# Kernel tuning notes

Measured on AMD Instinct MI355X. Metric: run time of the kernel, lower is better.

## Reference

```python
import jax, jax.numpy as jnp
import numpy as np

B, NV, JN = 1024, 8, 21
V = NV * JN            # 168 tokens = num_view * joint_num
F_DIM, NH, DQ, DV = 512, 4, 128, 128
HID = 512
EPS = 1e-6
NEG = float(-2**32 + 1)


def _layer_norm(x, g, b):
    mu = jnp.mean(x, axis=-1, keepdims=True)
    var = jnp.mean(jnp.square(x - mu), axis=-1, keepdims=True)
    return (x - mu) * jax.lax.rsqrt(var + EPS) * g + b


def setup_inputs() -> dict:
    key = jax.random.key(0)
    ks = jax.random.split(key, 12)
    s = 0.02
    return {
        "x": jax.random.normal(ks[0], (B, V, F_DIM), dtype=jnp.float32),
        "valid": jax.random.randint(ks[1], (B, NV), 0, 2),
        "wq": jax.random.normal(ks[2], (NH * DQ, F_DIM), dtype=jnp.float32) * s,
        "bq": jnp.zeros((NH * DQ,), dtype=jnp.float32),
        "wk": jax.random.normal(ks[3], (NH * DQ, F_DIM), dtype=jnp.float32) * s,
        "bk": jnp.zeros((NH * DQ,), dtype=jnp.float32),
        "wv": jax.random.normal(ks[4], (NH * DV, F_DIM), dtype=jnp.float32) * s,
        "bv": jnp.zeros((NH * DV,), dtype=jnp.float32),
        "fc_w": jax.random.normal(ks[5], (F_DIM, NH * DV), dtype=jnp.float32) * s,
        "fc_b": jnp.zeros((F_DIM,), dtype=jnp.float32),
        "ln1_g": jnp.ones((F_DIM,), dtype=jnp.float32),
        "ln1_b": jnp.zeros((F_DIM,), dtype=jnp.float32),
        "ln2_g": jnp.ones((F_DIM,), dtype=jnp.float32),
        "ln2_b": jnp.zeros((F_DIM,), dtype=jnp.float32),
        "fc1_w": jax.random.normal(ks[6], (HID, F_DIM), dtype=jnp.float32) * s,
        "fc1_b": jnp.zeros((HID,), dtype=jnp.float32),
        "fc2_w": jax.random.normal(ks[7], (F_DIM, HID), dtype=jnp.float32) * s,
        "fc2_b": jnp.zeros((F_DIM,), dtype=jnp.float32),
    }


def reference(x, valid, wq, bq, wk, bk, wv, bv, fc_w, fc_b,
              ln1_g, ln1_b, ln2_g, ln2_b, fc1_w, fc1_b, fc2_w, fc2_b):
    bs = x.shape[0]
    h = _layer_norm(x, ln1_g, ln1_b)                          # [B,V,f]
    q = (h @ wq.T + bq).reshape(bs, V, NH, DQ)                # [B,V,H,dq]
    k = (h @ wk.T + bk).reshape(bs, V, NH, DQ)
    v = (h @ wv.T + bv).reshape(bs, V, NH, DV)
    attn = jnp.einsum('bqhd,bkhd->bhqk', q, k) / jnp.sqrt(jnp.float32(DQ))
    # valid mask: per-view validity expanded to per-token, pairwise additive
    w = jnp.where(valid == 0, NEG, 0.0).astype(x.dtype)       # [B,NV]
    w = jnp.repeat(w, JN, axis=1)                             # [B,V], view-major
    m = w[:, :, None] + w[:, None, :]                         # [B,V,V]
    attn = attn + m[:, None, :, :]
    attn = jax.nn.softmax(attn, axis=-1)
    out = jnp.einsum('bhqk,bkhd->bqhd', attn, v).reshape(bs, V, NH * DV)
    out = out @ fc_w.T + fc_b
    x = x + out
    # MLP residual block
    h2 = _layer_norm(x, ln2_g, ln2_b)
    h2 = jax.nn.relu(h2 @ fc1_w.T + fc1_b) @ fc2_w.T + fc2_b
    return x + h2
```

## Files before the change

kernel.cpp:

```cpp
#include <hip/hip_runtime.h>
#include <stdint.h>

#define BATCH 1024
#define NVIEW 8
#define JN_   21
#define VTOK  168
#define FDIM  512
#define NHEAD 4
#define DHEAD 128
#define MROWS (BATCH*VTOK)
#define SCALE2 0.127517434f

typedef __attribute__((ext_vector_type(8))) short s8v;
typedef __attribute__((ext_vector_type(4))) short s4v;
typedef __attribute__((ext_vector_type(4))) float f4v;

static __device__ __forceinline__ short f2bf(float f){
  unsigned u = __builtin_bit_cast(unsigned, f);
  unsigned r = (u + 0x7FFFu + ((u >> 16) & 1u)) >> 16;
  return (short)(unsigned short)r;
}
static __device__ __forceinline__ float bf2f(short s){
  unsigned u = ((unsigned)(unsigned short)s) << 16;
  return __builtin_bit_cast(float, u);
}

#define GL16(gp, lp) __builtin_amdgcn_global_load_lds( \
    (__attribute__((address_space(1))) void*)(gp), \
    (__attribute__((address_space(3))) void*)(lp), 16, 0, 0)

__global__ __launch_bounds__(256) void convert_w(
    const float* __restrict__ wq, const float* __restrict__ wk,
    const float* __restrict__ wv, const float* __restrict__ fcw,
    const float* __restrict__ fc1, const float* __restrict__ fc2,
    short* __restrict__ dst){
  int id = blockIdx.x * 256 + threadIdx.x;
  int e = id * 4;
  int seg = e >> 18;
  int off = e & 262143;
  const float* s = seg==0?wq: seg==1?wk: seg==2?wv: seg==3?fcw: seg==4?fc1: fc2;
  float4 u = *(const float4*)(s + off);
  s4v o; o[0]=f2bf(u.x); o[1]=f2bf(u.y); o[2]=f2bf(u.z); o[3]=f2bf(u.w);
  *(s4v*)(dst + e) = o;
}

__global__ __launch_bounds__(256) void ln1_kernel(
    const float* __restrict__ x, const float* __restrict__ g,
    const float* __restrict__ bb, short* __restrict__ h){
  int row  = blockIdx.x * 4 + (threadIdx.x >> 6);
  int lane = threadIdx.x & 63;
  size_t base = (size_t)row * 512 + lane * 8;
  float4 u0 = *(const float4*)(x + base);
  float4 u1 = *(const float4*)(x + base + 4);
  float s = u0.x+u0.y+u0.z+u0.w + u1.x+u1.y+u1.z+u1.w;
  float q = u0.x*u0.x+u0.y*u0.y+u0.z*u0.z+u0.w*u0.w
          + u1.x*u1.x+u1.y*u1.y+u1.z*u1.z+u1.w*u1.w;
  #pragma unroll
  for (int o = 1; o < 64; o <<= 1){ s += __shfl_xor(s,o); q += __shfl_xor(q,o); }
  float mu = s * (1.f/512.f);
  float rstd = rsqrtf(q*(1.f/512.f) - mu*mu + 1e-6f);
  float4 g0 = *(const float4*)(g + lane*8),  g1 = *(const float4*)(g + lane*8 + 4);
  float4 b0 = *(const float4*)(bb + lane*8), b1 = *(const float4*)(bb + lane*8 + 4);
  s8v o_;
  o_[0]=f2bf((u0.x-mu)*rstd*g0.x+b0.x); o_[1]=f2bf((u0.y-mu)*rstd*g0.y+b0.y);
  o_[2]=f2bf((u0.z-mu)*rstd*g0.z+b0.z); o_[3]=f2bf((u0.w-mu)*rstd*g0.w+b0.w);
  o_[4]=f2bf((u1.x-mu)*rstd*g1.x+b1.x); o_[5]=f2bf((u1.y-mu)*rstd*g1.y+b1.y);
  o_[6]=f2bf((u1.z-mu)*rstd*g1.z+b1.z); o_[7]=f2bf((u1.w-mu)*rstd*g1.w+b1.w);
  *(s8v*)(h + base) = o_;
}

__global__ __launch_bounds__(256) void resid_ln(
    const float* __restrict__ x, const short* __restrict__ y,
    const float* __restrict__ g, const float* __restrict__ bb,
    short* __restrict__ g2){
  int row  = blockIdx.x * 4 + (threadIdx.x >> 6);
  int lane = threadIdx.x & 63;
  size_t base = (size_t)row * 512 + lane * 8;
  float4 u0 = *(const float4*)(x + base);
  float4 u1 = *(const float4*)(x + base + 4);
  s8v yv = *(const s8v*)(y + base);
  float v[8];
  v[0]=u0.x+bf2f(yv[0]); v[1]=u0.y+bf2f(yv[1]); v[2]=u0.z+bf2f(yv[2]); v[3]=u0.w+bf2f(yv[3]);
  v[4]=u1.x+bf2f(yv[4]); v[5]=u1.y+bf2f(yv[5]); v[6]=u1.z+bf2f(yv[6]); v[7]=u1.w+bf2f(yv[7]);
  float s = 0.f, q = 0.f;
  #pragma unroll
  for (int i = 0; i < 8; i++){ s += v[i]; q += v[i]*v[i]; }
  #pragma unroll
  for (int o = 1; o < 64; o <<= 1){ s += __shfl_xor(s,o); q += __shfl_xor(q,o); }
  float mu = s * (1.f/512.f);
  float rstd = rsqrtf(q*(1.f/512.f) - mu*mu + 1e-6f);
  float4 g0 = *(const float4*)(g + lane*8),  g1 = *(const float4*)(g + lane*8 + 4);
  float4 b0 = *(const float4*)(bb + lane*8), b1 = *(const float4*)(bb + lane*8 + 4);
  s8v o_;
  o_[0]=f2bf((v[0]-mu)*rstd*g0.x+b0.x); o_[1]=f2bf((v[1]-mu)*rstd*g0.y+b0.y);
  o_[2]=f2bf((v[2]-mu)*rstd*g0.z+b0.z); o_[3]=f2bf((v[3]-mu)*rstd*g0.w+b0.w);
  o_[4]=f2bf((v[4]-mu)*rstd*g1.x+b1.x); o_[5]=f2bf((v[5]-mu)*rstd*g1.y+b1.y);
  o_[6]=f2bf((v[6]-mu)*rstd*g1.z+b1.z); o_[7]=f2bf((v[7]-mu)*rstd*g1.w+b1.w);
  *(s8v*)(g2 + base) = o_;
}

template<int MODE>
__global__ __launch_bounds__(512) void gemm_bt(
    const short* __restrict__ A, const short* __restrict__ Bm,
    const float* __restrict__ bias0, const float* __restrict__ bias1,
    const float* __restrict__ aux, short* __restrict__ out0,
    short* __restrict__ out1, float* __restrict__ outf){
  __shared__ short As[3][16384];
  __shared__ short Bs[3][8192];
  int tid = threadIdx.x, lane = tid & 63;
  int wid = tid >> 6, wr = wid >> 1, wc = wid & 1;
  int lg = lane >> 4, l15 = lane & 15;
  int nwg  = gridDim.x * gridDim.y;
  int flat = blockIdx.y * gridDim.x + blockIdx.x;
  int cpx  = nwg >> 3;
  int swz  = (flat & 7) * cpx + (flat >> 3);
  int bx = swz % gridDim.x, by = swz / gridDim.x;
  size_t mt, nt;
  if (MODE == 1){ mt = bx; nt = by; }
  else          { nt = bx; mt = by; }
  size_t m0 = mt * 256, n0 = nt * 128;
  const short* Ab = A + m0 * 512;
  const short* Bb = Bm + n0 * 512;
  f4v zf = {0.f,0.f,0.f,0.f};
  f4v acc[4][4];
  #pragma unroll
  for (int m=0;m<4;m++)
    #pragma unroll
    for (int n=0;n<4;n++) acc[m][n] = zf;

#define STAGE_T(bufi, kt) do {                                        \
    _Pragma("unroll")                                                 \
    for (int r_ = 0; r_ < 4; r_++){                                   \
      int c_ = r_*512 + tid;                                          \
      int row_ = c_ >> 3;                                             \
      int chk_ = (c_ & 7) ^ (row_ & 7);                               \
      GL16(Ab + (size_t)row_*512 + (kt) + chk_*8, &As[bufi][c_*8]);   \
    }                                                                 \
    _Pragma("unroll")                                                 \
    for (int r_ = 0; r_ < 2; r_++){                                   \
      int c_ = r_*512 + tid;                                          \
      int row_ = c_ >> 3;                                             \
      int chk_ = (c_ & 7) ^ (row_ & 7);                               \
      GL16(Bb + (size_t)row_*512 + (kt) + chk_*8, &Bs[bufi][c_*8]);   \
    }                                                                 \
  } while(0)

  STAGE_T(0, 0); STAGE_T(1, 64); STAGE_T(2, 128);

  #pragma unroll
  for (int t = 0; t < 8; ++t){
    if (t < 6)       asm volatile("s_waitcnt vmcnt(12)" ::: "memory");
    else if (t == 6) asm volatile("s_waitcnt vmcnt(6)"  ::: "memory");
    else             asm volatile("s_waitcnt vmcnt(0)"  ::: "memory");
    __builtin_amdgcn_s_barrier();
    __builtin_amdgcn_sched_barrier(0);
    {
      const short* Ap = As[t % 3];
      const short* Bp = Bs[t % 3];
      #pragma unroll
      for (int kk8 = 0; kk8 < 8; kk8 += 4){
        s8v af_[4], bf_[4];
        int pc_ = ((kk8 + lg) ^ (l15 & 7)) << 3;
        #pragma unroll
        for (int m_=0;m_<4;m_++) af_[m_] = *(const s8v*)&Ap[(wr*64+m_*16+l15)*64 + pc_];
        #pragma unroll
        for (int n_=0;n_<4;n_++) bf_[n_] = *(const s8v*)&Bp[(wc*64+n_*16+l15)*64 + pc_];
        __builtin_amdgcn_s_setprio(1);
        #pragma unroll
        for (int m_=0;m_<4;m_++)
          #pragma unroll
          for (int n_=0;n_<4;n_++)
            acc[m_][n_] = __builtin_amdgcn_mfma_f32_16x16x32_bf16(af_[m_], bf_[n_], acc[m_][n_], 0,0,0);
        __builtin_amdgcn_s_setprio(0);
      }
    }
    if (t < 5){
      __builtin_amdgcn_s_barrier();
      __builtin_amdgcn_sched_barrier(0);
      STAGE_T((t + 3) % 3, (t + 3) * 64);
    }
  }
#undef STAGE_T

  #pragma unroll
  for (int m=0;m<4;m++)
  #pragma unroll
  for (int n=0;n<4;n++)
  #pragma unroll
  for (int r=0;r<4;r++){
    int rowL = wr*64 + m*16 + lg*4 + r;
    int colL = wc*64 + n*16 + l15;
    size_t gm = m0 + rowL, gn = n0 + colL;
    float val = acc[m][n][r];
    if (MODE == 0){
      int nn = (int)gn;
      val += (nn < 512) ? bias0[nn] : bias1[nn - 512];
      int head = (nn >> 7) & 3, d = nn & 127;
      size_t b = gm / 168, tok = gm - b * 168;
      size_t idx = ((b*4 + head)*168 + tok)*128 + d;
      ((nn < 512) ? out0 : out1)[idx] = f2bf(val);
    } else if (MODE == 1){
      val += bias0[gm];
      int hh = ((int)gm >> 7) & 3, d = (int)gm & 127;
      size_t b = gn / 168, tok = gn - b * 168;
      out0[((b*4 + hh)*128 + d)*168 + tok] = f2bf(val);
    } else if (MODE == 2 || MODE == 3){
      val += bias0[gn];
      if (MODE == 3) val = fmaxf(val, 0.f);
      out0[gm*512 + gn] = f2bf(val);
    } else {
      val += bias0[gn] + aux[gm*512 + gn] + bf2f(out1[gm*512 + gn]);
      outf[gm*512 + gn] = val;
    }
  }
}

__global__ __launch_bounds__(256, 2) void attn_kernel(
    const short* __restrict__ qg_, const short* __restrict__ kg_,
    const short* __restrict__ vtg_, const int* __restrict__ valid,
    short* __restrict__ outp){
  __shared__ short Ps[192*200];

  int tid = threadIdx.x, lane = tid & 63, wid = tid >> 6;
  int lg = lane >> 4, l15 = lane & 15;
  int bh = blockIdx.x, b = bh >> 2, hh = bh & 3;
  const short* qg  = qg_  + (size_t)bh * (168*128);
  const short* kg  = kg_  + (size_t)bh * (168*128);
  const short* vtg = vtg_ + (size_t)bh * (128*168);

  int bits = 0;
  #pragma unroll
  for (int v = 0; v < 8; v++) bits |= (valid[b*8 + v] != 0) << v;
  if (bits == 0) bits = 255;
  float wk2[11];
  #pragma unroll
  for (int n = 0; n < 11; n++){
    int kt = n*16 + l15;
    int view = (kt * 781) >> 14;
    wk2[n] = ((bits >> view) & 1) ? 0.0f : -1.0e9f;
  }

  int row0 = wid * 48;
  f4v zf = {0.f,0.f,0.f,0.f};

  s8v qf[3][4];
  #pragma unroll
  for (int m=0;m<3;m++)
    #pragma unroll
    for (int kf=0;kf<4;kf++)
      qf[m][kf] = *(const s8v*)(qg + (size_t)(row0 + m*16 + l15)*128 + kf*32 + lg*8);

  f4v accS[3][11];
  #pragma unroll
  for (int m=0;m<3;m++)
    #pragma unroll
    for (int n=0;n<11;n++) accS[m][n] = zf;
  s8v kb[2][4];
  #pragma unroll
  for (int kf=0;kf<4;kf++)
    kb[0][kf] = *(const s8v*)(kg + (size_t)l15*128 + kf*32 + lg*8);
  #pragma unroll
  for (int n=0;n<11;n++){
    if (n < 10){
      #pragma unroll
      for (int kf=0;kf<4;kf++)
        kb[(n+1)&1][kf] = *(const s8v*)(kg + (size_t)((n+1)*16 + l15)*128 + kf*32 + lg*8);
    }
    __builtin_amdgcn_s_setprio(1);
    #pragma unroll
    for (int kf=0;kf<4;kf++)
      #pragma unroll
      for (int m=0;m<3;m++)
        accS[m][n] = __builtin_amdgcn_mfma_f32_16x16x32_bf16(qf[m][kf], kb[n&1][kf], accS[m][n], 0,0,0);
    __builtin_amdgcn_s_setprio(0);
  }

  float inv_[3][4];
  #pragma unroll
  for (int m=0;m<3;m++){
    #pragma unroll
    for (int r=0;r<4;r++){
      int qtok = row0 + m*16 + lg*4 + r;
      float sum = 0.f;
      #pragma unroll
      for (int n=0;n<11;n++){
        float p = exp2f(fmaf(accS[m][n][r], SCALE2, wk2[n]));
        sum += p;
        Ps[qtok*200 + n*16 + l15] = f2bf(p);
      }
      sum += __shfl_xor(sum,1); sum += __shfl_xor(sum,2);
      sum += __shfl_xor(sum,4); sum += __shfl_xor(sum,8);
      inv_[m][r] = 1.0f / sum;
    }
  }
  {
    s8v z8 = {0,0,0,0,0,0,0,0};
    for (int i = lane; i < 96; i += 64){
      int rr = row0 + (i >> 1);
      *(s8v*)&Ps[rr*200 + 176 + (i&1)*8] = z8;
    }
  }

  s8v ap[3][6];
  #pragma unroll
  for (int m=0;m<3;m++)
    #pragma unroll
    for (int kf=0;kf<6;kf++)
      ap[m][kf] = *(const s8v*)&Ps[(row0 + m*16 + l15)*200 + kf*32 + lg*8];

  f4v accO[3][8];
  #pragma unroll
  for (int m=0;m<3;m++)
    #pragma unroll
    for (int n=0;n<8;n++) accO[m][n] = zf;
  s8v vb[2][6];
  #pragma unroll
  for (int kf=0;kf<6;kf++)
    vb[0][kf] = *(const s8v*)(vtg + (size_t)l15*168 + kf*32 + lg*8);
  #pragma unroll
  for (int n=0;n<8;n++){
    if (n < 7){
      #pragma unroll
      for (int kf=0;kf<6;kf++)
        vb[(n+1)&1][kf] = *(const s8v*)(vtg + (size_t)((n+1)*16 + l15)*168 + kf*32 + lg*8);
    }
    __builtin_amdgcn_s_setprio(1);
    #pragma unroll
    for (int kf=0;kf<6;kf++)
      #pragma unroll
      for (int m=0;m<3;m++)
        accO[m][n] = __builtin_amdgcn_mfma_f32_16x16x32_bf16(ap[m][kf], vb[n&1][kf], accO[m][n], 0,0,0);
    __builtin_amdgcn_s_setprio(0);
  }

  #pragma unroll
  for (int m=0;m<3;m++){
    #pragma unroll
    for (int r=0;r<4;r++){
      int qtok = row0 + m*16 + lg*4 + r;
      if (qtok < 168){
        float iv = inv_[m][r];
        size_t base = ((size_t)b*168 + qtok)*512 + hh*128;
        #pragma unroll
        for (int n=0;n<8;n++)
          outp[base + n*16 + l15] = f2bf(accO[m][n][r] * iv);
      }
    }
  }
}

extern "C" void kernel_launch(void* const* d_in, const int* in_sizes, int n_in,
                              void* d_out, int out_size, void* d_ws, size_t ws_size,
                              hipStream_t stream) {
  const float* x     = (const float*)d_in[0];
  const int*   valid = (const int*)  d_in[1];
  const float* wq    = (const float*)d_in[2];
  const float* bq    = (const float*)d_in[3];
  const float* wk    = (const float*)d_in[4];
  const float* bk    = (const float*)d_in[5];
  const float* wv    = (const float*)d_in[6];
  const float* bv    = (const float*)d_in[7];
  const float* fcw   = (const float*)d_in[8];
  const float* fcb   = (const float*)d_in[9];
  const float* ln1g  = (const float*)d_in[10];
  const float* ln1b  = (const float*)d_in[11];
  const float* ln2g  = (const float*)d_in[12];
  const float* ln2b  = (const float*)d_in[13];
  const float* fc1w  = (const float*)d_in[14];
  const float* fc1b  = (const float*)d_in[15];
  const float* fc2w  = (const float*)d_in[16];
  const float* fc2b  = (const float*)d_in[17];

  char* ws = (char*)d_ws;
  short* h       = (short*)(ws + 0LL);
  short* q_ws    = (short*)(ws + 176160768LL);
  short* k_ws    = (short*)(ws + 352321536LL);
  short* vt_ws   = (short*)(ws + 528482304LL);
  short* wb      = (short*)(ws + 704643072LL);
  short* attn_o  = h;
  short* y       = q_ws;
  short* g2      = h;
  short* a1      = k_ws;
  float* outp    = (float*)d_out;

  convert_w<<<1536, 256, 0, stream>>>(wq, wk, wv, fcw, fc1w, fc2w, wb);
  ln1_kernel<<<MROWS/4, 256, 0, stream>>>(x, ln1g, ln1b, h);
  gemm_bt<0><<<dim3(8, MROWS/256), 512, 0, stream>>>(h, wb, bq, bk, nullptr, q_ws, k_ws, nullptr);
  gemm_bt<1><<<dim3(2, MROWS/128), 512, 0, stream>>>(wb + 524288, h, bv, nullptr, nullptr, vt_ws, nullptr, nullptr);
  attn_kernel<<<BATCH*NHEAD, 256, 0, stream>>>(q_ws, k_ws, vt_ws, valid, attn_o);
  gemm_bt<2><<<dim3(4, MROWS/256), 512, 0, stream>>>(attn_o, wb + 786432, fcb, nullptr, nullptr, y, nullptr, nullptr);
  resid_ln<<<MROWS/4, 256, 0, stream>>>(x, y, ln2g, ln2b, g2);
  gemm_bt<3><<<dim3(4, MROWS/256), 512, 0, stream>>>(g2, wb + 1048576, fc1b, nullptr, nullptr, a1, nullptr, nullptr);
  gemm_bt<4><<<dim3(4, MROWS/256), 512, 0, stream>>>(a1, wb + 1310720, fc2b, nullptr, (float*)x, nullptr, y, outp);
}
```

Baseline: 1.527 ms.

## Keep full B panel in LDS and stream A fragments from global memory

Reworks the bf16 GEMM so each block loads its entire 128x512 weight panel into LDS once. A operands are then read directly from global memory into registers with double buffering, and the M tile doubles to 512 rows. This drops the triple-buffered A/B LDS pipeline and most barriers, and launch grids are adjusted to match. The trade-off is a large LDS footprint that limits occupancy, a latency-exposed upfront B load, and A reads that bypass LDS reuse.

```diff
diff --git a/kernel.cpp b/kernel.cpp
--- a/kernel.cpp
+++ b/kernel.cpp
@@ -100,13 +100,12 @@
 }
 
 template<int MODE>
-__global__ __launch_bounds__(512) void gemm_bt(
+__global__ __launch_bounds__(512, 2) void gemm_bt(
     const short* __restrict__ A, const short* __restrict__ Bm,
     const float* __restrict__ bias0, const float* __restrict__ bias1,
     const float* __restrict__ aux, short* __restrict__ out0,
     short* __restrict__ out1, float* __restrict__ outf){
-  __shared__ short As[3][16384];
-  __shared__ short Bs[3][8192];
+  __shared__ short Bs[128*512];
   int tid = threadIdx.x, lane = tid & 63;
   int wid = tid >> 6, wr = wid >> 1, wc = wid & 1;
   int lg = lane >> 4, l15 = lane & 15;
@@ -114,81 +113,64 @@
   int flat = blockIdx.y * gridDim.x + blockIdx.x;
   int cpx  = nwg >> 3;
   int swz  = (flat & 7) * cpx + (flat >> 3);
-  int bx = swz % gridDim.x, by = swz / gridDim.x;
   size_t mt, nt;
-  if (MODE == 1){ mt = bx; nt = by; }
-  else          { nt = bx; mt = by; }
-  size_t m0 = mt * 256, n0 = nt * 128;
-  const short* Ab = A + m0 * 512;
-  const short* Bb = Bm + n0 * 512;
+  if (MODE == 1){ mt = 0; nt = swz; }
+  else          { nt = swz % gridDim.x; mt = swz / gridDim.x; }
+  size_t m0 = mt * 512, n0 = nt * 128;
+
+  #pragma unroll
+  for (int i = 0; i < 16; i++){
+    int c = tid + i * 512;
+    int row = c >> 6, chk = c & 63;
+    int chs = (chk & ~7) | ((chk ^ row) & 7);
+    GL16(Bm + (size_t)(n0 + row)*512 + chs*8, &Bs[c*8]);
+  }
+  const short* Aw = A + (m0 + (size_t)wr*128 + l15)*512 + lg*8;
+  asm volatile("s_waitcnt vmcnt(0)" ::: "memory");
+  __builtin_amdgcn_s_barrier();
+
   f4v zf = {0.f,0.f,0.f,0.f};
-  f4v acc[4][4];
-  #pragma unroll
-  for (int m=0;m<4;m++)
+  f4v acc[8][4];
+  #pragma unroll
+  for (int m=0;m<8;m++)
     #pragma unroll
     for (int n=0;n<4;n++) acc[m][n] = zf;
 
-#define STAGE_T(bufi, kt) do {                                        \
-    _Pragma("unroll")                                                 \
-    for (int r_ = 0; r_ < 4; r_++){                                   \
-      int c_ = r_*512 + tid;                                          \
-      int row_ = c_ >> 3;                                             \
-      int chk_ = (c_ & 7) ^ (row_ & 7);                               \
-      GL16(Ab + (size_t)row_*512 + (kt) + chk_*8, &As[bufi][c_*8]);   \
-    }                                                                 \
-    _Pragma("unroll")                                                 \
-    for (int r_ = 0; r_ < 2; r_++){                                   \
-      int c_ = r_*512 + tid;                                          \
-      int row_ = c_ >> 3;                                             \
-      int chk_ = (c_ & 7) ^ (row_ & 7);                               \
-      GL16(Bb + (size_t)row_*512 + (kt) + chk_*8, &Bs[bufi][c_*8]);   \
-    }                                                                 \
-  } while(0)
-
-  STAGE_T(0, 0); STAGE_T(1, 64); STAGE_T(2, 128);
-
-  #pragma unroll
-  for (int t = 0; t < 8; ++t){
-    if (t < 6)       asm volatile("s_waitcnt vmcnt(12)" ::: "memory");
-    else if (t == 6) asm volatile("s_waitcnt vmcnt(6)"  ::: "memory");
-    else             asm volatile("s_waitcnt vmcnt(0)"  ::: "memory");
-    __builtin_amdgcn_s_barrier();
-    __builtin_amdgcn_sched_barrier(0);
+  s8v a[2][8];
+  #pragma unroll
+  for (int m=0;m<8;m++) a[0][m] = *(const s8v*)(Aw + m*16*512);
+  #pragma unroll
+  for (int ks = 0; ks < 16; ks++){
+    const int cur = ks & 1;
+    if (ks < 15){
+      #pragma unroll
+      for (int m=0;m<8;m++)
+        a[cur^1][m] = *(const s8v*)(Aw + m*16*512 + (ks+1)*32);
+    }
+    s8v bfr[4];
     {
-      const short* Ap = As[t % 3];
-      const short* Bp = Bs[t % 3];
-      #pragma unroll
-      for (int kk8 = 0; kk8 < 8; kk8 += 4){
-        s8v af_[4], bf_[4];
-        int pc_ = ((kk8 + lg) ^ (l15 & 7)) << 3;
-        #pragma unroll
-        for (int m_=0;m_<4;m_++) af_[m_] = *(const s8v*)&Ap[(wr*64+m_*16+l15)*64 + pc_];
-        #pragma unroll
-        for (int n_=0;n_<4;n_++) bf_[n_] = *(const s8v*)&Bp[(wc*64+n_*16+l15)*64 + pc_];
-        __builtin_amdgcn_s_setprio(1);
-        #pragma unroll
-        for (int m_=0;m_<4;m_++)
-          #pragma unroll
-          for (int n_=0;n_<4;n_++)
-            acc[m_][n_] = __builtin_amdgcn_mfma_f32_16x16x32_bf16(af_[m_], bf_[n_], acc[m_][n_], 0,0,0);
-        __builtin_amdgcn_s_setprio(0);
-      }
-    }
-    if (t < 5){
-      __builtin_amdgcn_s_barrier();
-      __builtin_amdgcn_sched_barrier(0);
-      STAGE_T((t + 3) % 3, (t + 3) * 64);
-    }
-  }
-#undef STAGE_T
-
-  #pragma unroll
-  for (int m=0;m<4;m++)
+      int lowv = ((4*(ks&1) + lg) ^ l15) & 7;
+      int chs8 = (((ks >> 1) << 3) + lowv) * 8;
+      #pragma unroll
+      for (int n=0;n<4;n++)
+        bfr[n] = *(const s8v*)&Bs[(wc*64 + n*16 + l15)*512 + chs8];
+    }
+    __builtin_amdgcn_s_setprio(1);
+    #pragma unroll
+    for (int m=0;m<8;m++)
+      #pragma unroll
+      for (int n=0;n<4;n++)
+        acc[m][n] = __builtin_amdgcn_mfma_f32_16x16x32_bf16(a[cur][m], bfr[n], acc[m][n], 0,0,0);
+    __builtin_amdgcn_s_setprio(0);
+  }
+
+  #pragma unroll
+  for (int m=0;m<8;m++)
   #pragma unroll
   for (int n=0;n<4;n++)
   #pragma unroll
   for (int r=0;r<4;r++){
-    int rowL = wr*64 + m*16 + lg*4 + r;
+    int rowL = wr*128 + m*16 + lg*4 + r;
     int colL = wc*64 + n*16 + l15;
     size_t gm = m0 + rowL, gn = n0 + colL;
     float val = acc[m][n][r];
@@ -385,11 +367,11 @@
 
   convert_w<<<1536, 256, 0, stream>>>(wq, wk, wv, fcw, fc1w, fc2w, wb);
   ln1_kernel<<<MROWS/4, 256, 0, stream>>>(x, ln1g, ln1b, h);
-  gemm_bt<0><<<dim3(8, MROWS/256), 512, 0, stream>>>(h, wb, bq, bk, nullptr, q_ws, k_ws, nullptr);
-  gemm_bt<1><<<dim3(2, MROWS/128), 512, 0, stream>>>(wb + 524288, h, bv, nullptr, nullptr, vt_ws, nullptr, nullptr);
+  gemm_bt<0><<<dim3(8, MROWS/512), 512, 0, stream>>>(h, wb, bq, bk, nullptr, q_ws, k_ws, nullptr);
+  gemm_bt<1><<<dim3(MROWS/128, 1), 512, 0, stream>>>(wb + 524288, h, bv, nullptr, nullptr, vt_ws, nullptr, nullptr);
   attn_kernel<<<BATCH*NHEAD, 256, 0, stream>>>(q_ws, k_ws, vt_ws, valid, attn_o);
-  gemm_bt<2><<<dim3(4, MROWS/256), 512, 0, stream>>>(attn_o, wb + 786432, fcb, nullptr, nullptr, y, nullptr, nullptr);
+  gemm_bt<2><<<dim3(4, MROWS/512), 512, 0, stream>>>(attn_o, wb + 786432, fcb, nullptr, nullptr, y, nullptr, nullptr);
   resid_ln<<<MROWS/4, 256, 0, stream>>>(x, y, ln2g, ln2b, g2);
-  gemm_bt<3><<<dim3(4, MROWS/256), 512, 0, stream>>>(g2, wb + 1048576, fc1b, nullptr, nullptr, a1, nullptr, nullptr);
-  gemm_bt<4><<<dim3(4, MROWS/256), 512, 0, stream>>>(a1, wb + 1310720, fc2b, nullptr, (float*)x, nullptr, y, outp);
-}
+  gemm_bt<3><<<dim3(4, MROWS/512), 512, 0, stream>>>(g2, wb + 1048576, fc1b, nullptr, nullptr, a1, nullptr, nullptr);
+  gemm_bt<4><<<dim3(4, MROWS/512), 512, 0, stream>>>(a1, wb + 1310720, fc2b, nullptr, (float*)x, nullptr, y, outp);
+}
```

New measurement: 1.878 ms. 23.0% more time.
